# Kernel optimization log

Hardware: AMD Instinct MI355X
Metric: run time of the kernel (lower is better)

## Reference

```python
import jax, jax.numpy as jnp
import numpy as np

H, N, DIN, DOUT = 8, 2048, 768, 1024
HD = DOUT // H
SCALE = 1.0 / float(np.sqrt(HD))
NEG = -1e9
EPS = 1e-5


def setup_inputs() -> dict:
    key = jax.random.key(0)
    ks = jax.random.split(key, 20)
    w = lambda i, shape: jax.random.normal(ks[i], shape, jnp.float32) * 0.02
    inp = {
        'x': jax.random.normal(ks[0], (N, DIN), jnp.float32),
        'batch': jnp.sort(jax.random.randint(ks[1], (N,), 0, 64)).astype(jnp.int64)
                 if jax.config.jax_enable_x64 else jnp.sort(jax.random.randint(ks[1], (N,), 0, 64)),
        'motif_to_atom_attn': jax.random.normal(ks[2], (H, N, N), jnp.float32),
        'wq_w': w(3, (DIN, DOUT)), 'wq_b': jnp.zeros((DOUT,), jnp.float32),
        'wk_w': w(4, (DIN, DOUT)), 'wk_b': jnp.zeros((DOUT,), jnp.float32),
        'wv_w': w(5, (DIN, DOUT)), 'wv_b': jnp.zeros((DOUT,), jnp.float32),
        'wo_w': w(6, (DOUT, DIN)), 'wo_b': jnp.zeros((DIN,), jnp.float32),
        'ln_g': jnp.ones((DIN,), jnp.float32), 'ln_b': jnp.zeros((DIN,), jnp.float32),
        'alpha': jnp.float32(0.5), 'beta': jnp.float32(0.5),
        'gate_q_w': w(7, (DOUT, H)), 'gate_q_b': jnp.zeros((H,), jnp.float32),
        'gate_k_w': w(8, (DOUT, H)), 'gate_k_b': jnp.zeros((H,), jnp.float32),
        'head_interaction': jnp.eye(H, dtype=jnp.float32) + 0.01 * jax.random.normal(ks[9], (H, H), jnp.float32),
    }
    return inp


def reference(x, batch, motif_to_atom_attn, wq_w, wq_b, wk_w, wk_b, wv_w, wv_b,
              wo_w, wo_b, ln_g, ln_b, alpha, beta, gate_q_w, gate_q_b,
              gate_k_w, gate_k_b, head_interaction):
    n = x.shape[0]
    # projections -> [H, N, hd]
    q = (x @ wq_w + wq_b).reshape(n, H, HD).transpose(1, 0, 2)
    k = (x @ wk_w + wk_b).reshape(n, H, HD).transpose(1, 0, 2)
    v = (x @ wv_w + wv_b).reshape(n, H, HD).transpose(1, 0, 2)
    # scaled scores with block-diagonal batch mask [H, N, N]
    scores = jnp.einsum('hid,hjd->hij', q, k) * SCALE
    mask = batch[:, None] == batch[None, :]
    scores = jnp.where(mask[None, :, :], scores, NEG)
    attn_final = scores
    # Guide bias: torch permutes (N,N,H)->permute(2,1,0) which TRANSPOSES node dims
    attn_base = alpha * scores + beta * motif_to_atom_attn          # [H, N, N]
    attn_final = attn_final + jnp.swapaxes(attn_base, 1, 2)        # transposed in (i,j)
    # dynamic gating
    q_flat = q.transpose(1, 0, 2).reshape(n, DOUT)
    k_flat = k.transpose(1, 0, 2).reshape(n, DOUT)
    gq = jnp.tanh(q_flat @ gate_q_w + gate_q_b)                    # [N, H]
    gk = jnp.tanh(k_flat @ gate_k_w + gate_k_b)                    # [N, H]
    attn_final = attn_final + scores * (gq.T[:, :, None] + gk.T[:, None, :])
    # head interaction: res[m,i,j] = sum_h scores[h,i,j] * W[h,m]
    attn_final = attn_final + jnp.einsum('hij,hm->mij', scores, head_interaction)
    probs = jax.nn.softmax(attn_final, axis=-1)
    out = jnp.einsum('hij,hjd->hid', probs, v).transpose(1, 0, 2).reshape(n, DOUT)
    out = out @ wo_w + wo_b
    y = out + x
    mu = jnp.mean(y, axis=-1, keepdims=True)
    var = jnp.mean(jnp.square(y - mu), axis=-1, keepdims=True)
    y = (y - mu) * jax.lax.rsqrt(var + EPS) * ln_g + ln_b
    return y, attn_final
```

## Files before the change

### kernel.cpp

```cpp
#include <hip/hip_runtime.h>

#define NN    2048
#define DIN   768
#define DOUT  1024
#define NH    8
#define HD    128
#define SCALEF 0.08838834764831845f
#define NEGF  (-1.0e9f)
#define EPSF  1e-5f
#define EXPSHIFT 16.0f

typedef __attribute__((ext_vector_type(4))) float f32x4;
typedef __attribute__((ext_vector_type(8))) short bf16x8;

#define OFF_OBF  0
#define OFF_WOT  1048576
#define OFF_YACC 1441792
#define OFF_Q    3686400
#define OFF_K    4734976
#define OFF_VB   5783552
#define OFF_VT   6832128
#define OFF_XB   7880704
#define OFF_WT   8667136
#define OFF_GQ   9846784
#define OFF_GK   9863168

__device__ __forceinline__ short f2bf(float f) {
  union { float f; unsigned u; } v; v.f = f;
  unsigned r = v.u + 0x7FFF + ((v.u >> 16) & 1);
  return (short)(r >> 16);
}
__device__ __forceinline__ float bf2f(short s) {
  union { unsigned u; float f; } v; v.u = ((unsigned)(unsigned short)s) << 16;
  return v.f;
}

__global__ __launch_bounds__(256) void k_prep(const float* __restrict__ x,
                                              short* __restrict__ xb,
                                              const float* __restrict__ wq,
                                              const float* __restrict__ wk,
                                              const float* __restrict__ wv,
                                              short* __restrict__ Wt,
                                              const float* __restrict__ wo,
                                              short* __restrict__ wot) {
  const int bid = blockIdx.x;
  const int tid = threadIdx.x;
  if (bid < 1536) {
    int idx = bid * 256 + tid;
    float4 v = ((const float4*)x)[idx];
    union { short s[4]; float2 f; } u;
    u.s[0] = f2bf(v.x); u.s[1] = f2bf(v.y); u.s[2] = f2bf(v.z); u.s[3] = f2bf(v.w);
    ((float2*)xb)[idx] = u.f;
    return;
  }
  __shared__ float t[64][65];
  if (bid < 2112) {
    const int w = bid - 1536;
    const int z = w / 192, rem = w % 192;
    const int c0 = (rem % 16) * 64, k0 = (rem / 16) * 64;
    const float* Wm = (z == 0) ? wq : (z == 1) ? wk : wv;
#pragma unroll
    for (int l = 0; l < 4; ++l) {
      int f = tid + l * 256;
      int r = f >> 4, c4 = (f & 15) * 4;
      *(float4*)&t[r][c4] = *(const float4*)(Wm + (size_t)(k0 + r) * DOUT + c0 + c4);
    }
    __syncthreads();
    int r2 = tid >> 2, q = tid & 3;
    union { short s[16]; float4 f[2]; } buf;
#pragma unroll
    for (int jj = 0; jj < 16; ++jj) buf.s[jj] = f2bf(t[q * 16 + jj][r2]);
    short* dst = Wt + (size_t)z * (1024 * 768) + (size_t)(c0 + r2) * 768 + k0 + q * 16;
    ((float4*)dst)[0] = buf.f[0];
    ((float4*)dst)[1] = buf.f[1];
  } else {
    const int w = bid - 2112;
    const int c0 = (w % 12) * 64, k0 = (w / 12) * 64;
#pragma unroll
    for (int l = 0; l < 4; ++l) {
      int f = tid + l * 256;
      int r = f >> 4, c4 = (f & 15) * 4;
      *(float4*)&t[r][c4] = *(const float4*)(wo + (size_t)(k0 + r) * DIN + c0 + c4);
    }
    __syncthreads();
    int r2 = tid >> 2, q = tid & 3;
    union { short s[16]; float4 f[2]; } buf;
#pragma unroll
    for (int jj = 0; jj < 16; ++jj) buf.s[jj] = f2bf(t[q * 16 + jj][r2]);
    short* dst = wot + (size_t)(c0 + r2) * DOUT + k0 + q * 16;
    ((float4*)dst)[0] = buf.f[0];
    ((float4*)dst)[1] = buf.f[1];
  }
}

__global__ __launch_bounds__(256) void k_qkv(const short* __restrict__ xb,
                                             const short* __restrict__ Wt,
                                             const float* __restrict__ bq,
                                             const float* __restrict__ bk,
                                             const float* __restrict__ bv,
                                             short* __restrict__ Qb,
                                             short* __restrict__ Kb,
                                             short* __restrict__ Vb) {
  const int n0 = blockIdx.x * 128;
  const int i0 = blockIdx.y * 128;
  const int mat = n0 >> 10;
  const int cl = n0 & 1023;
  const float* bias = (mat == 0) ? bq : (mat == 1) ? bk : bv;
  const short* Wm = Wt + (size_t)mat * (1024 * 768);
  const int tid = threadIdx.x, lane = tid & 63, wave = tid >> 6;
  const int ln = lane & 15, quad = lane >> 4, q8 = quad * 8;
  f32x4 acc[2][8];
#pragma unroll
  for (int a = 0; a < 2; ++a)
#pragma unroll
    for (int b = 0; b < 8; ++b) acc[a][b] = (f32x4){0.f, 0.f, 0.f, 0.f};
  const short* a0 = xb + (size_t)(i0 + 32 * wave + ln) * DIN + q8;
  const short* a1 = a0 + 16 * DIN;
  const short* bp = Wm + (size_t)(cl + ln) * DIN + q8;
  for (int ks = 0; ks < 24; ++ks) {
    bf16x8 A0 = *(const bf16x8*)(a0 + 32 * ks);
    bf16x8 A1 = *(const bf16x8*)(a1 + 32 * ks);
#pragma unroll
    for (int nt = 0; nt < 8; ++nt) {
      bf16x8 B = *(const bf16x8*)(bp + (size_t)nt * (16 * DIN) + 32 * ks);
      acc[0][nt] = __builtin_amdgcn_mfma_f32_16x16x32_bf16(A0, B, acc[0][nt], 0, 0, 0);
      acc[1][nt] = __builtin_amdgcn_mfma_f32_16x16x32_bf16(A1, B, acc[1][nt], 0, 0, 0);
    }
  }
#pragma unroll
  for (int rt = 0; rt < 2; ++rt)
#pragma unroll
    for (int nt = 0; nt < 8; ++nt) {
      int cg = cl + 16 * nt + ln;
      float bb = bias[cg];
#pragma unroll
      for (int reg = 0; reg < 4; ++reg) {
        int rr = i0 + 32 * wave + 16 * rt + quad * 4 + reg;
        short s = f2bf(acc[rt][nt][reg] + bb);
        if (mat == 2) {
          Vb[(size_t)rr * 1024 + cg] = s;
        } else {
          int h = cg >> 7, d = cg & 127;
          (mat == 0 ? Qb : Kb)[((size_t)h * NN + rr) * HD + d] = s;
        }
      }
    }
}

__global__ __launch_bounds__(256) void k_vtg(const short* __restrict__ Qb,
                                             const short* __restrict__ Kb,
                                             const float* __restrict__ gqw,
                                             const float* __restrict__ gqb,
                                             const float* __restrict__ gkw,
                                             const float* __restrict__ gkb,
                                             float* __restrict__ GQ,
                                             float* __restrict__ GK,
                                             const short* __restrict__ Vb,
                                             short* __restrict__ Vt) {
  const int bid = blockIdx.x;
  const int tid = threadIdx.x;
  __shared__ __align__(16) char smem[17408];
  if (bid < 2048) {
    auto red8 = (float (*)[256])(smem);
    const int i = bid;
    float aq[NH] = {}, ak[NH] = {};
    for (int d = tid; d < DOUT; d += 256) {
      int h = d >> 7, dd = d & 127;
      float qv = bf2f(Qb[((size_t)h * NN + i) * HD + dd]);
      float kv = bf2f(Kb[((size_t)h * NN + i) * HD + dd]);
#pragma unroll
      for (int h2 = 0; h2 < NH; ++h2) {
        aq[h2] = fmaf(qv, gqw[d * NH + h2], aq[h2]);
        ak[h2] = fmaf(kv, gkw[d * NH + h2], ak[h2]);
      }
    }
#pragma unroll
    for (int h = 0; h < NH; ++h) red8[h][tid] = aq[h];
    __syncthreads();
    for (int s = 128; s > 0; s >>= 1) {
      if (tid < s) {
#pragma unroll
        for (int h = 0; h < NH; ++h) red8[h][tid] += red8[h][tid + s];
      }
      __syncthreads();
    }
    if (tid < NH) GQ[i * NH + tid] = tanhf(red8[tid][0] + gqb[tid]);
    __syncthreads();
#pragma unroll
    for (int h = 0; h < NH; ++h) red8[h][tid] = ak[h];
    __syncthreads();
    for (int s = 128; s > 0; s >>= 1) {
      if (tid < s) {
#pragma unroll
        for (int h = 0; h < NH; ++h) red8[h][tid] += red8[h][tid + s];
      }
      __syncthreads();
    }
    if (tid < NH) GK[i * NH + tid] = tanhf(red8[tid][0] + gkb[tid]);
  } else {
    auto t = (short (*)[136])(smem);
    const int w = bid - 2048;
    const int i0 = (w & 31) * 64, h = w >> 5;
#pragma unroll
    for (int l = 0; l < 2; ++l) {
      int f = tid + l * 256;
      int r = f >> 3, c8 = (f & 7) * 16;
      const short* src = Vb + (size_t)(i0 + r) * 1024 + h * HD + c8;
      *(bf16x8*)&t[r][c8] = *(const bf16x8*)src;
      *(bf16x8*)&t[r][c8 + 8] = *(const bf16x8*)(src + 8);
    }
    __syncthreads();
    int d = tid >> 1, half = tid & 1;
    union { short s[32]; float4 f[4]; } buf;
#pragma unroll
    for (int ii = 0; ii < 32; ++ii) buf.s[ii] = t[32 * half + ii][d];
    short* dst = Vt + (size_t)h * (HD * NN) + (size_t)d * NN + i0 + 32 * half;
#pragma unroll
    for (int q = 0; q < 4; ++q) ((float4*)dst)[q] = buf.f[q];
  }
}

__global__ __launch_bounds__(256, 4) void k_sa(const short* __restrict__ Qb,
                                               const short* __restrict__ Kb,
                                               const int* __restrict__ batch,
                                               const float* __restrict__ motif,
                                               const float* __restrict__ GQ,
                                               const float* __restrict__ GK,
                                               const float* __restrict__ Wh,
                                               const float* __restrict__ alpha_p,
                                               const float* __restrict__ beta_p,
                                               float* __restrict__ ATTN) {
  const unsigned gid = blockIdx.y * gridDim.x + blockIdx.x;
  const unsigned xcd = gid & 7, idx = gid >> 3;
  const unsigned P = xcd + 8 * (idx >> 8);
  const unsigned r256 = idx & 255;
  const unsigned bx = 16 * (P & 3) + (r256 & 15);
  const unsigned by = 16 * (P >> 2) + (r256 >> 4);
  const int i0 = by * 32, j0 = bx * 32;

  const int tid = threadIdx.x, lane = tid & 63, wave = tid >> 6;
  const int wr = wave >> 1, wc = wave & 1;
  const int ln = lane & 15, quad = lane >> 4, q8 = quad * 8;

  __shared__ __align__(16) char smem[38400];
  auto Qs  = (short (*)[32][136])(smem);
  auto Ks  = (short (*)[32][136])(smem + 17408);
  auto oL  = (float (*)[36])(smem);
  auto gqL = (float (*)[12])(smem + 34816);
  auto gkL = (float (*)[12])(smem + 36352);
  float* sW = (float*)(smem + 37888);

  const int rA = 16 * wr + quad * 4;
  const int cA = 16 * wc + ln;

  const int srow = tid >> 3, sseg = (tid & 7) * 16;
  const short* gQ0 = Qb + (size_t)(i0 + srow) * HD + sseg;
  const short* gK0 = Kb + (size_t)(j0 + srow) * HD + sseg;
  const size_t hstep = (size_t)NN * HD;

  {
    bf16x8 q0 = *(const bf16x8*)(gQ0);
    bf16x8 q1 = *(const bf16x8*)(gQ0 + 8);
    bf16x8 k0 = *(const bf16x8*)(gK0);
    bf16x8 k1 = *(const bf16x8*)(gK0 + 8);
    *(bf16x8*)&Qs[0][srow][sseg] = q0;
    *(bf16x8*)&Qs[0][srow][sseg + 8] = q1;
    *(bf16x8*)&Ks[0][srow][sseg] = k0;
    *(bf16x8*)&Ks[0][srow][sseg + 8] = k1;
  }
  bf16x8 cq0 = *(const bf16x8*)(gQ0 + hstep);
  bf16x8 cq1 = *(const bf16x8*)(gQ0 + hstep + 8);
  bf16x8 ck0 = *(const bf16x8*)(gK0 + hstep);
  bf16x8 ck1 = *(const bf16x8*)(gK0 + hstep + 8);
  if (tid < 64) {
    const int half = tid >> 5, r = tid & 31;
    const float* src = (half ? GK : GQ) + (size_t)((half ? j0 : i0) + r) * NH;
    float4 a = *(const float4*)src;
    float4 b = *(const float4*)(src + 4);
    float* dst = half ? &gkL[r][0] : &gqL[r][0];
    *(float4*)dst = a;
    *(float4*)(dst + 4) = b;
    sW[tid] = Wh[tid];
  }
  const int4 bi4 = *(const int4*)(batch + i0 + rA);
  const int bj = batch[j0 + cA];
  const float alpha = alpha_p[0], beta = beta_p[0];
  __syncthreads();

  f32x4 accS[NH], accT[NH];
#pragma unroll
  for (int h = 0; h < NH; ++h) {
    accS[h] = (f32x4){0.f, 0.f, 0.f, 0.f};
    accT[h] = (f32x4){0.f, 0.f, 0.f, 0.f};
  }

#pragma unroll
  for (int h = 0; h < NH; ++h) {
    const int bufc = h & 1;
    bf16x8 nq0, nq1, nk0, nk1;
    if (h < 6) {
      const short* gq_ = gQ0 + (size_t)(h + 2) * hstep;
      const short* gk_ = gK0 + (size_t)(h + 2) * hstep;
      nq0 = *(const bf16x8*)(gq_);
      nq1 = *(const bf16x8*)(gq_ + 8);
      nk0 = *(const bf16x8*)(gk_);
      nk1 = *(const bf16x8*)(gk_ + 8);
    }
#pragma unroll
    for (int ks = 0; ks < 4; ++ks) {
      bf16x8 aS = *(const bf16x8*)&Qs[bufc][16 * wr + ln][ks * 32 + q8];
      bf16x8 bS = *(const bf16x8*)&Ks[bufc][16 * wc + ln][ks * 32 + q8];
      accS[h] = __builtin_amdgcn_mfma_f32_16x16x32_bf16(aS, bS, accS[h], 0, 0, 0);
      bf16x8 aT = *(const bf16x8*)&Ks[bufc][16 * wr + ln][ks * 32 + q8];
      bf16x8 bT = *(const bf16x8*)&Qs[bufc][16 * wc + ln][ks * 32 + q8];
      accT[h] = __builtin_amdgcn_mfma_f32_16x16x32_bf16(aT, bT, accT[h], 0, 0, 0);
    }
    if (h < 7) {
      *(bf16x8*)&Qs[bufc ^ 1][srow][sseg] = cq0;
      *(bf16x8*)&Qs[bufc ^ 1][srow][sseg + 8] = cq1;
      *(bf16x8*)&Ks[bufc ^ 1][srow][sseg] = ck0;
      *(bf16x8*)&Ks[bufc ^ 1][srow][sseg + 8] = ck1;
    }
    __syncthreads();
    if (h < 6) { cq0 = nq0; cq1 = nq1; ck0 = nk0; ck1 = nk1; }
  }

  int okm[4];
  okm[0] = (bi4.x == bj); okm[1] = (bi4.y == bj);
  okm[2] = (bi4.z == bj); okm[3] = (bi4.w == bj);
#pragma unroll
  for (int reg = 0; reg < 4; ++reg)
#pragma unroll
    for (int h = 0; h < NH; ++h)
      accS[h][reg] = okm[reg] ? accS[h][reg] * SCALEF : NEGF;

  const int orow = tid >> 3, oslot = (tid & 7) * 4;
  union { float4 v; float f[4]; } moc, mon, mo2;
  moc.v = *(const float4*)(motif + ((size_t)(j0 + cA)) * NN + i0 + rA);
  mon.v = *(const float4*)(motif + ((size_t)(NN + j0 + cA)) * NN + i0 + rA);
#pragma unroll
  for (int h = 0; h < NH; ++h) {
    if (h < 6)
      mo2.v = *(const float4*)(motif + ((size_t)(h + 2) * NN + j0 + cA) * NN + i0 + rA);
    float w8[NH];
#pragma unroll
    for (int h2 = 0; h2 < NH; ++h2) w8[h2] = sW[h2 * NH + h];
    const float gkj = gkL[cA][h];
#pragma unroll
    for (int reg = 0; reg < 4; ++reg) {
      float tv = okm[reg] ? accT[h][reg] * SCALEF : NEGF;
      float hm = 0.f;
#pragma unroll
      for (int h2 = 0; h2 < NH; ++h2) hm = fmaf(accS[h2][reg], w8[h2], hm);
      float o = accS[h][reg] * (1.f + gqL[rA + reg][h] + gkj) +
                alpha * tv + beta * moc.f[reg] + hm;
      oL[rA + reg][cA] = o;
    }
    __syncthreads();
    float4 ov = *(const float4*)&oL[orow][oslot];
    *(float4*)(ATTN + ((size_t)h * NN + i0 + orow) * NN + j0 + oslot) = ov;
    if (h < 7) __syncthreads();
    moc.v = mon.v;
    mon.v = mo2.v;
  }
}

__global__ __launch_bounds__(256) void k_pv(const float* __restrict__ ATTN,
                                            const short* __restrict__ Vt,
                                            short* __restrict__ Obf) {
  const int bid = blockIdx.x;
  const int h = bid & 7;
  const int i0 = (bid >> 3) * 16;
  const int tid = threadIdx.x, lane = tid & 63, wave = tid >> 6;
  const int ln = lane & 15, quad = lane >> 4, q8 = quad * 8;
  __shared__ float accL[4][16][140];
  __shared__ float SUML[4][16];
  const int jbase = wave * 512;
  const float* arow = ATTN + ((size_t)h * NN + i0 + ln) * NN + jbase;
  const short* vbase = Vt + (size_t)h * (HD * NN) + jbase;
  f32x4 acc[8];
#pragma unroll
  for (int nt = 0; nt < 8; ++nt) acc[nt] = (f32x4){0.f, 0.f, 0.f, 0.f};
  float rowsum = 0.f;
  for (int c = 0; c < 16; ++c) {
    const int jk = c * 32;
    float4 u1 = *(const float4*)(arow + jk + q8);
    float4 u2 = *(const float4*)(arow + jk + q8 + 4);
    float p0 = __expf(u1.x - EXPSHIFT), p1 = __expf(u1.y - EXPSHIFT);
    float p2 = __expf(u1.z - EXPSHIFT), p3 = __expf(u1.w - EXPSHIFT);
    float p4 = __expf(u2.x - EXPSHIFT), p5 = __expf(u2.y - EXPSHIFT);
    float p6 = __expf(u2.z - EXPSHIFT), p7 = __expf(u2.w - EXPSHIFT);
    rowsum += ((p0 + p1) + (p2 + p3)) + ((p4 + p5) + (p6 + p7));
    bf16x8 a;
    a[0] = f2bf(p0); a[1] = f2bf(p1); a[2] = f2bf(p2); a[3] = f2bf(p3);
    a[4] = f2bf(p4); a[5] = f2bf(p5); a[6] = f2bf(p6); a[7] = f2bf(p7);
#pragma unroll
    for (int nt = 0; nt < 8; ++nt) {
      bf16x8 b = *(const bf16x8*)(vbase + (size_t)(16 * nt + ln) * NN + jk + q8);
      acc[nt] = __builtin_amdgcn_mfma_f32_16x16x32_bf16(a, b, acc[nt], 0, 0, 0);
    }
  }
  rowsum += __shfl_xor(rowsum, 16);
  rowsum += __shfl_xor(rowsum, 32);
  if (lane < 16) SUML[wave][ln] = rowsum;
#pragma unroll
  for (int nt = 0; nt < 8; ++nt)
#pragma unroll
    for (int reg = 0; reg < 4; ++reg)
      accL[wave][quad * 4 + reg][16 * nt + ln] = acc[nt][reg];
  __syncthreads();
  const int r = tid >> 4, d0 = (tid & 15) * 8;
  const float inv = 1.0f / (SUML[0][r] + SUML[1][r] + SUML[2][r] + SUML[3][r]);
  union { short s[8]; bf16x8 v; } ob;
#pragma unroll
  for (int e = 0; e < 8; ++e) {
    float s = accL[0][r][d0 + e] + accL[1][r][d0 + e] +
              accL[2][r][d0 + e] + accL[3][r][d0 + e];
    ob.s[e] = f2bf(s * inv);
  }
  *(bf16x8*)(Obf + (size_t)(i0 + r) * DOUT + h * HD + d0) = ob.v;
}

__global__ __launch_bounds__(256) void k_outproj(const short* __restrict__ Obf,
                                                 const short* __restrict__ wot,
                                                 float* __restrict__ YACC) {
  const int n0 = blockIdx.x * 128;
  const int i0 = blockIdx.y * 64;
  const int tid = threadIdx.x, lane = tid & 63, wave = tid >> 6;
  const int ln = lane & 15, quad = lane >> 4, q8 = quad * 8;
  f32x4 acc[8];
#pragma unroll
  for (int nt = 0; nt < 8; ++nt) acc[nt] = (f32x4){0.f, 0.f, 0.f, 0.f};
  const short* a0 = Obf + (size_t)(i0 + 16 * wave + ln) * DOUT + q8;
  const short* bp = wot + (size_t)(n0 + ln) * DOUT + q8;
  for (int ks = 0; ks < 32; ++ks) {
    bf16x8 A0 = *(const bf16x8*)(a0 + 32 * ks);
#pragma unroll
    for (int nt = 0; nt < 8; ++nt) {
      bf16x8 B = *(const bf16x8*)(bp + (size_t)nt * (16 * DOUT) + 32 * ks);
      acc[nt] = __builtin_amdgcn_mfma_f32_16x16x32_bf16(A0, B, acc[nt], 0, 0, 0);
    }
  }
#pragma unroll
  for (int nt = 0; nt < 8; ++nt) {
    int cg = n0 + 16 * nt + ln;
#pragma unroll
    for (int reg = 0; reg < 4; ++reg) {
      int rr = i0 + 16 * wave + quad * 4 + reg;
      YACC[(size_t)rr * DIN + cg] = acc[nt][reg];
    }
  }
}

__global__ __launch_bounds__(256) void k_ln(const float* __restrict__ YACC,
                                            const float* __restrict__ x,
                                            const float* __restrict__ wo_b,
                                            const float* __restrict__ g,
                                            const float* __restrict__ b,
                                            float* __restrict__ y) {
  const int i = blockIdx.x;
  const int tid = threadIdx.x;
  float v[3];
#pragma unroll
  for (int t = 0; t < 3; ++t) {
    int cc = tid + t * 256;
    v[t] = YACC[(size_t)i * DIN + cc] + wo_b[cc] + x[(size_t)i * DIN + cc];
  }
  __shared__ float red[256];
  red[tid] = v[0] + v[1] + v[2];
  __syncthreads();
  for (int s = 128; s > 0; s >>= 1) {
    if (tid < s) red[tid] += red[tid + s];
    __syncthreads();
  }
  const float mu = red[0] * (1.0f / DIN);
  __syncthreads();
  float q = 0.f;
#pragma unroll
  for (int t = 0; t < 3; ++t) {
    float d = v[t] - mu;
    q += d * d;
  }
  red[tid] = q;
  __syncthreads();
  for (int s = 128; s > 0; s >>= 1) {
    if (tid < s) red[tid] += red[tid + s];
    __syncthreads();
  }
  const float rs = rsqrtf(red[0] * (1.0f / DIN) + EPSF);
#pragma unroll
  for (int t = 0; t < 3; ++t) {
    int cc = tid + t * 256;
    y[(size_t)i * DIN + cc] = (v[t] - mu) * rs * g[cc] + b[cc];
  }
}

extern "C" void kernel_launch(void* const* d_in, const int* in_sizes, int n_in,
                              void* d_out, int out_size, void* d_ws, size_t ws_size,
                              hipStream_t stream) {
  (void)in_sizes; (void)n_in; (void)out_size; (void)ws_size;
  const float* x       = (const float*)d_in[0];
  const int*   batch   = (const int*)d_in[1];
  const float* motif   = (const float*)d_in[2];
  const float* wq_w    = (const float*)d_in[3];
  const float* wq_b    = (const float*)d_in[4];
  const float* wk_w    = (const float*)d_in[5];
  const float* wk_b    = (const float*)d_in[6];
  const float* wv_w    = (const float*)d_in[7];
  const float* wv_b    = (const float*)d_in[8];
  const float* wo_w    = (const float*)d_in[9];
  const float* wo_b    = (const float*)d_in[10];
  const float* ln_g    = (const float*)d_in[11];
  const float* ln_b    = (const float*)d_in[12];
  const float* alpha_p = (const float*)d_in[13];
  const float* beta_p  = (const float*)d_in[14];
  const float* gq_w    = (const float*)d_in[15];
  const float* gq_b    = (const float*)d_in[16];
  const float* gk_w    = (const float*)d_in[17];
  const float* gk_b    = (const float*)d_in[18];
  const float* headW   = (const float*)d_in[19];

  float* y    = (float*)d_out;
  float* ATTN = (float*)d_out + (size_t)NN * DIN;
  float* ws   = (float*)d_ws;
  short* Obf  = (short*)(ws + OFF_OBF);
  short* wot  = (short*)(ws + OFF_WOT);
  float* YACC = ws + OFF_YACC;
  short* Qb   = (short*)(ws + OFF_Q);
  short* Kb   = (short*)(ws + OFF_K);
  short* Vb   = (short*)(ws + OFF_VB);
  short* Vt   = (short*)(ws + OFF_VT);
  short* xb   = (short*)(ws + OFF_XB);
  short* Wt   = (short*)(ws + OFF_WT);
  float* GQ   = ws + OFF_GQ;
  float* GK   = ws + OFF_GK;

  k_prep<<<2304, 256, 0, stream>>>(x, xb, wq_w, wk_w, wv_w, Wt, wo_w, wot);
  k_qkv<<<dim3(24, 16), 256, 0, stream>>>(xb, Wt, wq_b, wk_b, wv_b, Qb, Kb, Vb);
  k_vtg<<<2304, 256, 0, stream>>>(Qb, Kb, gq_w, gq_b, gk_w, gk_b, GQ, GK, Vb, Vt);
  k_sa<<<dim3(64, 64), 256, 0, stream>>>(Qb, Kb, batch, motif, GQ, GK, headW,
                                         alpha_p, beta_p, ATTN);
  k_pv<<<1024, 256, 0, stream>>>(ATTN, Vt, Obf);
  k_outproj<<<dim3(6, 32), 256, 0, stream>>>(Obf, wot, YACC);
  k_ln<<<NN, 256, 0, stream>>>(YACC, x, wo_b, ln_g, ln_b, y);
}
```

Before: 552.7 us.

## Stage GEMM weight tiles in LDS, shrink tiles, use wave-shuffle reductions

```diff
diff --git a/kernel.cpp b/kernel.cpp
--- a/kernel.cpp
+++ b/kernel.cpp
@@ -102,49 +102,65 @@
                                              short* __restrict__ Kb,
                                              short* __restrict__ Vb) {
   const int n0 = blockIdx.x * 128;
-  const int i0 = blockIdx.y * 128;
+  const int i0 = blockIdx.y * 64;
   const int mat = n0 >> 10;
   const int cl = n0 & 1023;
   const float* bias = (mat == 0) ? bq : (mat == 1) ? bk : bv;
   const short* Wm = Wt + (size_t)mat * (1024 * 768);
   const int tid = threadIdx.x, lane = tid & 63, wave = tid >> 6;
   const int ln = lane & 15, quad = lane >> 4, q8 = quad * 8;
-  f32x4 acc[2][8];
-#pragma unroll
-  for (int a = 0; a < 2; ++a)
-#pragma unroll
-    for (int b = 0; b < 8; ++b) acc[a][b] = (f32x4){0.f, 0.f, 0.f, 0.f};
-  const short* a0 = xb + (size_t)(i0 + 32 * wave + ln) * DIN + q8;
-  const short* a1 = a0 + 16 * DIN;
-  const short* bp = Wm + (size_t)(cl + ln) * DIN + q8;
+  __shared__ __align__(16) short Bs[2][128][56];
+  const int brow = tid >> 1, bseg = (tid & 1) * 16;
+  const short* gB = Wm + (size_t)(cl + brow) * DIN + bseg;
+  {
+    bf16x8 b0 = *(const bf16x8*)(gB);
+    bf16x8 b1 = *(const bf16x8*)(gB + 8);
+    *(bf16x8*)&Bs[0][brow][bseg] = b0;
+    *(bf16x8*)&Bs[0][brow][bseg + 8] = b1;
+  }
+  bf16x8 cb0 = *(const bf16x8*)(gB + 32);
+  bf16x8 cb1 = *(const bf16x8*)(gB + 40);
+  __syncthreads();
+  f32x4 acc[8];
+#pragma unroll
+  for (int nt = 0; nt < 8; ++nt) acc[nt] = (f32x4){0.f, 0.f, 0.f, 0.f};
+  const short* a0 = xb + (size_t)(i0 + 16 * wave + ln) * DIN + q8;
   for (int ks = 0; ks < 24; ++ks) {
+    const int bufc = ks & 1;
+    bf16x8 nb0, nb1;
+    if (ks < 22) {
+      nb0 = *(const bf16x8*)(gB + 32 * (ks + 2));
+      nb1 = *(const bf16x8*)(gB + 32 * (ks + 2) + 8);
+    }
     bf16x8 A0 = *(const bf16x8*)(a0 + 32 * ks);
-    bf16x8 A1 = *(const bf16x8*)(a1 + 32 * ks);
 #pragma unroll
     for (int nt = 0; nt < 8; ++nt) {
-      bf16x8 B = *(const bf16x8*)(bp + (size_t)nt * (16 * DIN) + 32 * ks);
-      acc[0][nt] = __builtin_amdgcn_mfma_f32_16x16x32_bf16(A0, B, acc[0][nt], 0, 0, 0);
-      acc[1][nt] = __builtin_amdgcn_mfma_f32_16x16x32_bf16(A1, B, acc[1][nt], 0, 0, 0);
-    }
-  }
-#pragma unroll
-  for (int rt = 0; rt < 2; ++rt)
-#pragma unroll
-    for (int nt = 0; nt < 8; ++nt) {
-      int cg = cl + 16 * nt + ln;
-      float bb = bias[cg];
-#pragma unroll
-      for (int reg = 0; reg < 4; ++reg) {
-        int rr = i0 + 32 * wave + 16 * rt + quad * 4 + reg;
-        short s = f2bf(acc[rt][nt][reg] + bb);
-        if (mat == 2) {
-          Vb[(size_t)rr * 1024 + cg] = s;
-        } else {
-          int h = cg >> 7, d = cg & 127;
-          (mat == 0 ? Qb : Kb)[((size_t)h * NN + rr) * HD + d] = s;
-        }
+      bf16x8 B = *(const bf16x8*)&Bs[bufc][16 * nt + ln][q8];
+      acc[nt] = __builtin_amdgcn_mfma_f32_16x16x32_bf16(A0, B, acc[nt], 0, 0, 0);
+    }
+    if (ks < 23) {
+      *(bf16x8*)&Bs[bufc ^ 1][brow][bseg] = cb0;
+      *(bf16x8*)&Bs[bufc ^ 1][brow][bseg + 8] = cb1;
+    }
+    __syncthreads();
+    if (ks < 22) { cb0 = nb0; cb1 = nb1; }
+  }
+#pragma unroll
+  for (int nt = 0; nt < 8; ++nt) {
+    int cg = cl + 16 * nt + ln;
+    float bb = bias[cg];
+#pragma unroll
+    for (int reg = 0; reg < 4; ++reg) {
+      int rr = i0 + 16 * wave + quad * 4 + reg;
+      short s = f2bf(acc[nt][reg] + bb);
+      if (mat == 2) {
+        Vb[(size_t)rr * 1024 + cg] = s;
+      } else {
+        int h = cg >> 7, d = cg & 127;
+        (mat == 0 ? Qb : Kb)[((size_t)h * NN + rr) * HD + d] = s;
       }
     }
+  }
 }
 
 __global__ __launch_bounds__(256) void k_vtg(const short* __restrict__ Qb,
@@ -161,42 +177,48 @@
   const int tid = threadIdx.x;
   __shared__ __align__(16) char smem[17408];
   if (bid < 2048) {
-    auto red8 = (float (*)[256])(smem);
     const int i = bid;
+    const int lane = tid & 63, wave = tid >> 6;
     float aq[NH] = {}, ak[NH] = {};
     for (int d = tid; d < DOUT; d += 256) {
       int h = d >> 7, dd = d & 127;
       float qv = bf2f(Qb[((size_t)h * NN + i) * HD + dd]);
       float kv = bf2f(Kb[((size_t)h * NN + i) * HD + dd]);
-#pragma unroll
-      for (int h2 = 0; h2 < NH; ++h2) {
-        aq[h2] = fmaf(qv, gqw[d * NH + h2], aq[h2]);
-        ak[h2] = fmaf(kv, gkw[d * NH + h2], ak[h2]);
+      float4 ga = *(const float4*)(gqw + (size_t)d * NH);
+      float4 gb = *(const float4*)(gqw + (size_t)d * NH + 4);
+      float4 ha = *(const float4*)(gkw + (size_t)d * NH);
+      float4 hb = *(const float4*)(gkw + (size_t)d * NH + 4);
+      aq[0] = fmaf(qv, ga.x, aq[0]); aq[1] = fmaf(qv, ga.y, aq[1]);
+      aq[2] = fmaf(qv, ga.z, aq[2]); aq[3] = fmaf(qv, ga.w, aq[3]);
+      aq[4] = fmaf(qv, gb.x, aq[4]); aq[5] = fmaf(qv, gb.y, aq[5]);
+      aq[6] = fmaf(qv, gb.z, aq[6]); aq[7] = fmaf(qv, gb.w, aq[7]);
+      ak[0] = fmaf(kv, ha.x, ak[0]); ak[1] = fmaf(kv, ha.y, ak[1]);
+      ak[2] = fmaf(kv, ha.z, ak[2]); ak[3] = fmaf(kv, ha.w, ak[3]);
+      ak[4] = fmaf(kv, hb.x, ak[4]); ak[5] = fmaf(kv, hb.y, ak[5]);
+      ak[6] = fmaf(kv, hb.z, ak[6]); ak[7] = fmaf(kv, hb.w, ak[7]);
+    }
+#pragma unroll
+    for (int h = 0; h < NH; ++h) {
+#pragma unroll
+      for (int off = 1; off < 64; off <<= 1) {
+        aq[h] += __shfl_xor(aq[h], off);
+        ak[h] += __shfl_xor(ak[h], off);
       }
     }
-#pragma unroll
-    for (int h = 0; h < NH; ++h) red8[h][tid] = aq[h];
-    __syncthreads();
-    for (int s = 128; s > 0; s >>= 1) {
-      if (tid < s) {
-#pragma unroll
-        for (int h = 0; h < NH; ++h) red8[h][tid] += red8[h][tid + s];
+    auto part = (float (*)[16])(smem);
+    if (lane == 0) {
+#pragma unroll
+      for (int h = 0; h < NH; ++h) {
+        part[wave][h] = aq[h];
+        part[wave][8 + h] = ak[h];
       }
-      __syncthreads();
-    }
-    if (tid < NH) GQ[i * NH + tid] = tanhf(red8[tid][0] + gqb[tid]);
-    __syncthreads();
-#pragma unroll
-    for (int h = 0; h < NH; ++h) red8[h][tid] = ak[h];
-    __syncthreads();
-    for (int s = 128; s > 0; s >>= 1) {
-      if (tid < s) {
-#pragma unroll
-        for (int h = 0; h < NH; ++h) red8[h][tid] += red8[h][tid + s];
-      }
-      __syncthreads();
-    }
-    if (tid < NH) GK[i * NH + tid] = tanhf(red8[tid][0] + gkb[tid]);
+    }
+    __syncthreads();
+    if (tid < 16) {
+      float s = part[0][tid] + part[1][tid] + part[2][tid] + part[3][tid];
+      if (tid < 8) GQ[(size_t)i * NH + tid] = tanhf(s + gqb[tid]);
+      else GK[(size_t)i * NH + tid - 8] = tanhf(s + gkb[tid - 8]);
+    }
   } else {
     auto t = (short (*)[136])(smem);
     const int w = bid - 2048;
@@ -424,25 +446,39 @@
 __global__ __launch_bounds__(256) void k_outproj(const short* __restrict__ Obf,
                                                  const short* __restrict__ wot,
                                                  float* __restrict__ YACC) {
-  const int n0 = blockIdx.x * 128;
+  const int n0 = blockIdx.x * 64;
   const int i0 = blockIdx.y * 64;
   const int tid = threadIdx.x, lane = tid & 63, wave = tid >> 6;
   const int ln = lane & 15, quad = lane >> 4, q8 = quad * 8;
-  f32x4 acc[8];
-#pragma unroll
-  for (int nt = 0; nt < 8; ++nt) acc[nt] = (f32x4){0.f, 0.f, 0.f, 0.f};
+  __shared__ __align__(16) short Bs[2][64][56];
+  const int brow = tid >> 2, bseg = (tid & 3) * 8;
+  const short* gB = wot + (size_t)(n0 + brow) * DOUT + bseg;
+  {
+    bf16x8 b0 = *(const bf16x8*)(gB);
+    *(bf16x8*)&Bs[0][brow][bseg] = b0;
+  }
+  bf16x8 cb0 = *(const bf16x8*)(gB + 32);
+  __syncthreads();
+  f32x4 acc[4];
+#pragma unroll
+  for (int nt = 0; nt < 4; ++nt) acc[nt] = (f32x4){0.f, 0.f, 0.f, 0.f};
   const short* a0 = Obf + (size_t)(i0 + 16 * wave + ln) * DOUT + q8;
-  const short* bp = wot + (size_t)(n0 + ln) * DOUT + q8;
   for (int ks = 0; ks < 32; ++ks) {
+    const int bufc = ks & 1;
+    bf16x8 nb0;
+    if (ks < 30) nb0 = *(const bf16x8*)(gB + 32 * (ks + 2));
     bf16x8 A0 = *(const bf16x8*)(a0 + 32 * ks);
 #pragma unroll
-    for (int nt = 0; nt < 8; ++nt) {
-      bf16x8 B = *(const bf16x8*)(bp + (size_t)nt * (16 * DOUT) + 32 * ks);
+    for (int nt = 0; nt < 4; ++nt) {
+      bf16x8 B = *(const bf16x8*)&Bs[bufc][16 * nt + ln][q8];
       acc[nt] = __builtin_amdgcn_mfma_f32_16x16x32_bf16(A0, B, acc[nt], 0, 0, 0);
     }
-  }
-#pragma unroll
-  for (int nt = 0; nt < 8; ++nt) {
+    if (ks < 31) *(bf16x8*)&Bs[bufc ^ 1][brow][bseg] = cb0;
+    __syncthreads();
+    if (ks < 30) cb0 = nb0;
+  }
+#pragma unroll
+  for (int nt = 0; nt < 4; ++nt) {
     int cg = n0 + 16 * nt + ln;
 #pragma unroll
     for (int reg = 0; reg < 4; ++reg) {
@@ -460,34 +496,31 @@
                                             float* __restrict__ y) {
   const int i = blockIdx.x;
   const int tid = threadIdx.x;
+  const int lane = tid & 63, wave = tid >> 6;
   float v[3];
 #pragma unroll
   for (int t = 0; t < 3; ++t) {
     int cc = tid + t * 256;
     v[t] = YACC[(size_t)i * DIN + cc] + wo_b[cc] + x[(size_t)i * DIN + cc];
   }
-  __shared__ float red[256];
-  red[tid] = v[0] + v[1] + v[2];
+  __shared__ float p1[4], p2[4];
+  float s = v[0] + v[1] + v[2];
+#pragma unroll
+  for (int off = 1; off < 64; off <<= 1) s += __shfl_xor(s, off);
+  if (lane == 0) p1[wave] = s;
   __syncthreads();
-  for (int s = 128; s > 0; s >>= 1) {
-    if (tid < s) red[tid] += red[tid + s];
-    __syncthreads();
-  }
-  const float mu = red[0] * (1.0f / DIN);
-  __syncthreads();
+  const float mu = (p1[0] + p1[1] + p1[2] + p1[3]) * (1.0f / DIN);
   float q = 0.f;
 #pragma unroll
   for (int t = 0; t < 3; ++t) {
     float d = v[t] - mu;
     q += d * d;
   }
-  red[tid] = q;
+#pragma unroll
+  for (int off = 1; off < 64; off <<= 1) q += __shfl_xor(q, off);
+  if (lane == 0) p2[wave] = q;
   __syncthreads();
-  for (int s = 128; s > 0; s >>= 1) {
-    if (tid < s) red[tid] += red[tid + s];
-    __syncthreads();
-  }
-  const float rs = rsqrtf(red[0] * (1.0f / DIN) + EPSF);
+  const float rs = rsqrtf((p2[0] + p2[1] + p2[2] + p2[3]) * (1.0f / DIN) + EPSF);
 #pragma unroll
   for (int t = 0; t < 3; ++t) {
     int cc = tid + t * 256;
@@ -536,11 +569,11 @@
   float* GK   = ws + OFF_GK;
 
   k_prep<<<2304, 256, 0, stream>>>(x, xb, wq_w, wk_w, wv_w, Wt, wo_w, wot);
-  k_qkv<<<dim3(24, 16), 256, 0, stream>>>(xb, Wt, wq_b, wk_b, wv_b, Qb, Kb, Vb);
+  k_qkv<<<dim3(24, 32), 256, 0, stream>>>(xb, Wt, wq_b, wk_b, wv_b, Qb, Kb, Vb);
   k_vtg<<<2304, 256, 0, stream>>>(Qb, Kb, gq_w, gq_b, gk_w, gk_b, GQ, GK, Vb, Vt);
   k_sa<<<dim3(64, 64), 256, 0, stream>>>(Qb, Kb, batch, motif, GQ, GK, headW,
                                          alpha_p, beta_p, ATTN);
   k_pv<<<1024, 256, 0, stream>>>(ATTN, Vt, Obf);
-  k_outproj<<<dim3(6, 32), 256, 0, stream>>>(Obf, wot, YACC);
+  k_outproj<<<dim3(12, 32), 256, 0, stream>>>(Obf, wot, YACC);
   k_ln<<<NN, 256, 0, stream>>>(YACC, x, wo_b, ln_g, ln_b, y);
 }
```

Result: faster. 454.5 us (-17.8%).
